# Performance work log

Measured on AMD Instinct MI355X. Metric: run time of the kernel, lower is better.

Reference implementation:

```python
import jax, jax.numpy as jnp
import numpy as np

N = 100000   # nodes
E = 1600000  # edges
H = 128      # hidden_dim
B = 4096     # number of root pairs
HOPS = 3


def setup_inputs() -> dict:
    key = jax.random.key(0)
    ks = jax.random.split(key, 12)
    s = 0.05
    return {
        "node_feat": jax.random.normal(ks[0], (N, H), jnp.float32),
        "send_embd": jax.random.normal(ks[1], (N, H), jnp.float32),
        "edge_index": jax.random.randint(ks[2], (2, E), 0, N, dtype=jnp.int32),
        "root_index": jax.random.randint(ks[3], (2 * B,), 0, N, dtype=jnp.int32),
        "agg_by_source": 1,
        "lin1_W": jax.random.normal(ks[4], (2 * H, H), jnp.float32) * s,
        "lin1_b": jnp.zeros((H,), jnp.float32),
        "gat_W": jax.random.normal(ks[5], (HOPS, H, H), jnp.float32) * s,
        "gat_asrc": jax.random.normal(ks[6], (HOPS, H), jnp.float32) * s,
        "gat_adst": jax.random.normal(ks[7], (HOPS, H), jnp.float32) * s,
        "gat_b": jnp.zeros((HOPS, H), jnp.float32),
        "lstm_Wih": jax.random.normal(ks[8], (HOPS, 2 * H, 4 * H), jnp.float32) * s,
        "lstm_Whh": jax.random.normal(ks[9], (HOPS, H, 4 * H), jnp.float32) * s,
        "lstm_b": jnp.zeros((HOPS, 4 * H), jnp.float32),
        "lin2_W": jax.random.normal(ks[10], (H, H), jnp.float32) * s,
        "lin2_b": jnp.zeros((H,), jnp.float32),
    }


def _gat_breadth(x, src, dst, W, a_src, a_dst, b):
    # GATConv(heads=1) followed by tanh (GeniePath Breadth layer)
    xw = x @ W                                  # [N, H]
    e_score = jax.nn.leaky_relu((xw @ a_src)[src] + (xw @ a_dst)[dst], 0.2)  # [E]
    # softmax over incoming edges of each destination node
    m = jax.ops.segment_max(e_score, dst, num_segments=N)
    ex = jnp.exp(e_score - m[dst])
    z = jax.ops.segment_sum(ex, dst, num_segments=N)
    alpha = ex / z[dst]                          # [E]
    agg = jax.ops.segment_sum(alpha[:, None] * xw[src], dst, num_segments=N)
    return jnp.tanh(agg + b)


def _lstm_step(inp, h, c, Wih, Whh, b):
    gates = inp @ Wih + h @ Whh + b              # [N, 4H]
    i, f, g, o = jnp.split(gates, 4, axis=-1)
    c = jax.nn.sigmoid(f) * c + jax.nn.sigmoid(i) * jnp.tanh(g)
    h = jax.nn.sigmoid(o) * jnp.tanh(c)
    return h, c


def reference(node_feat, send_embd, edge_index, root_index, agg_by_source,
              lin1_W, lin1_b, gat_W, gat_asrc, gat_adst, gat_b,
              lstm_Wih, lstm_Whh, lstm_b, lin2_W, lin2_b):
    src, dst = edge_index[0], edge_index[1]
    # Aggregation stage input: concat node embedding with broadcast embedding
    x = jnp.concatenate([node_feat, send_embd], axis=1) @ lin1_W + lin1_b  # [N, H]
    # GeniePathLazy: all breadth (GAT) layers run on the projected input x
    h_tmps = [
        _gat_breadth(x, src, dst, gat_W[i], gat_asrc[i], gat_adst[i], gat_b[i])
        for i in range(HOPS)
    ]
    # Depth: per-node LSTM over the hop axis, input = cat(h_tmp, x_prev)
    h = jnp.zeros_like(x)
    c = jnp.zeros_like(x)
    xs = x
    for i in range(HOPS):
        inp = jnp.concatenate([h_tmps[i], xs], axis=1)   # [N, 2H]
        h, c = _lstm_step(inp, h, c, lstm_Wih[i], lstm_Whh[i], lstm_b[i])
        xs = h
    out = xs @ lin2_W + lin2_b                            # [N, H]
    roots = root_index.reshape(-1, 2)
    src_nodes = roots[:, 0] if agg_by_source else roots[:, 1]
    return out[src_nodes]                                 # [B, H]
```

## Files before the change

### kernel.cpp

```cpp
#include <hip/hip_runtime.h>

constexpr int N  = 100000;
constexpr int E  = 1600000;
constexpr int H  = 128;
constexpr int NB = 4096;
constexpr int HOPS = 3;
constexpr int EPT = 8;

constexpr int WOFF_L1  = 0;
constexpr int WOFF_GAT = 32768;
constexpr int WOFF_CAT = 81920;
constexpr int WOFF_L2  = 671744;
constexpr int WTOT     = 688128;

constexpr size_t ALIGN = 256;
constexpr size_t alup(size_t x) { return (x + ALIGN - 1) & ~(ALIGN - 1); }

constexpr size_t OFF_X       = 0;
constexpr size_t OFF_SSRC    = alup(OFF_X + (size_t)N * H * 4);
constexpr size_t OFF_SDST    = alup(OFF_SSRC + (size_t)3 * N * 4);
constexpr size_t OFF_WVEC    = alup(OFF_SDST + (size_t)3 * N * 4);
constexpr size_t OFF_SELMAP  = alup(OFF_WVEC + 6 * H * 4);
constexpr size_t OFF_NODELST = alup(OFF_SELMAP + (size_t)N * 4);
constexpr size_t OFF_CNT     = alup(OFF_NODELST + NB * 4);
constexpr size_t OFF_DEG     = alup(OFF_CNT + 256);
constexpr size_t OFF_OFFS    = alup(OFF_DEG + NB * 4);
constexpr size_t OFF_CURSOR  = alup(OFF_OFFS + (NB + 1) * 4);
constexpr size_t OFF_ESORT   = alup(OFF_CURSOR + NB * 4);
constexpr size_t OFF_AGGXH   = alup(OFF_ESORT + (size_t)E * 4);
constexpr size_t OFF_AGGXL   = alup(OFF_AGGXH + (size_t)3 * NB * H * 2);
constexpr size_t OFF_XSH     = alup(OFF_AGGXL + (size_t)3 * NB * H * 2);
constexpr size_t OFF_XSL     = alup(OFF_XSH + (size_t)NB * H * 2);
constexpr size_t OFF_HH      = alup(OFF_XSL + (size_t)NB * H * 2);
constexpr size_t OFF_HL      = alup(OFF_HH + (size_t)NB * H * 2);
constexpr size_t OFF_CBUF    = alup(OFF_HL + (size_t)NB * H * 2);
constexpr size_t OFF_L2OUT   = alup(OFF_CBUF + (size_t)NB * H * 4);
constexpr size_t OFF_WHI     = alup(OFF_L2OUT + (size_t)NB * H * 4);
constexpr size_t OFF_WLO     = alup(OFF_WHI + (size_t)WTOT * 2);

constexpr size_t OFF_AGGRAW  = OFF_X;
constexpr size_t OFF_WV2     = OFF_X + (size_t)16 * 1024 * 1024;
constexpr size_t OFF_C2      = OFF_WV2 + 6 * 256 * 4;

__device__ __forceinline__ float lrelu(float v) { return v > 0.f ? v : 0.2f * v; }
__device__ __forceinline__ float sigmoidf_(float v) { return 1.f / (1.f + __expf(-v)); }

__device__ __forceinline__ unsigned short f2bf(float f) {
  unsigned u = __float_as_uint(f);
  unsigned r = (u + 0x7FFFu + ((u >> 16) & 1u)) >> 16;
  return (unsigned short)r;
}
__device__ __forceinline__ float bf2f(unsigned short h) {
  return __uint_as_float((unsigned)h << 16);
}
__device__ __forceinline__ void split_rne(float f, unsigned short& hi, unsigned short& lo) {
  unsigned short hh = f2bf(f);
  hi = hh;
  lo = f2bf(f - bf2f(hh));
}
__device__ __forceinline__ void split_trunc(float f, short* hi, short* lo) {
  unsigned u = __float_as_uint(f);
  *hi = (short)(u >> 16);
  float r = f - __uint_as_float(u & 0xFFFF0000u);
  *lo = (short)(__float_as_uint(r) >> 16);
}

typedef short bf16x8 __attribute__((ext_vector_type(8)));
typedef float f32x4  __attribute__((ext_vector_type(4)));

#define MFMA3(ACC, AH, AL, BH, BL)                                               \
  ACC = __builtin_amdgcn_mfma_f32_16x16x32_bf16(AH, BH, ACC, 0, 0, 0);           \
  ACC = __builtin_amdgcn_mfma_f32_16x16x32_bf16(AH, BL, ACC, 0, 0, 0);           \
  ACC = __builtin_amdgcn_mfma_f32_16x16x32_bf16(AL, BH, ACC, 0, 0, 0);

__global__ void init_ws(int* __restrict__ sel_map, int* __restrict__ deg,
                        int* __restrict__ cursor, int* __restrict__ cnt,
                        float* __restrict__ cbuf, unsigned short* __restrict__ hh,
                        unsigned short* __restrict__ hl, int* __restrict__ need_flag) {
  int i = blockIdx.x * 256 + threadIdx.x;
  int stride = gridDim.x * 256;
  for (int n = i; n < N; n += stride) { sel_map[n] = -1; need_flag[n] = 0; }
  for (int n = i; n < NB; n += stride) { deg[n] = 0; cursor[n] = 0; }
  if (i < 64) cnt[i] = 0;
  for (int n = i; n < NB * H; n += stride) { cbuf[n] = 0.f; hh[n] = 0; hl[n] = 0; }
}

__global__ void prep_kernel(const float* __restrict__ gat_W,
                            const float* __restrict__ a_src,
                            const float* __restrict__ a_dst,
                            float* __restrict__ wvec,
                            const float* __restrict__ lin1_W,
                            const float* __restrict__ Wih,
                            const float* __restrict__ Whh,
                            const float* __restrict__ lin2_W,
                            unsigned short* __restrict__ whi,
                            unsigned short* __restrict__ wlo) {
  if (blockIdx.x < 6) {
    int i = blockIdx.x >> 1, which = blockIdx.x & 1;
    int k = threadIdx.x;
    __shared__ float av[H];
    if (k < H) av[k] = which ? a_dst[i * H + k] : a_src[i * H + k];
    __syncthreads();
    if (k >= H) return;
    const float* Wr = gat_W + (size_t)i * H * H + (size_t)k * H;
    float s = 0.f;
    #pragma unroll 8
    for (int j = 0; j < H; j++) s = fmaf(Wr[j], av[j], s);
    wvec[(i * 2 + which) * H + k] = s;
    return;
  }
  int idx = (blockIdx.x - 6) * 256 + threadIdx.x;
  if (idx >= WTOT) return;
  float v;
  if (idx < WOFF_GAT) {
    int rel = idx;
    int e = rel & 7, lane = (rel >> 3) & 63, tile = rel >> 9;
    int nl = lane & 15, quad = lane >> 4;
    int c = tile & 7, t = tile >> 3;
    int n = c * 16 + nl, k = t * 32 + quad * 8 + e;
    v = lin1_W[k * 128 + n];
  } else if (idx < WOFF_CAT) {
    int rel = idx - WOFF_GAT;
    int hop = rel / 16384; rel %= 16384;
    int e = rel & 7, lane = (rel >> 3) & 63, tile = rel >> 9;
    int nl = lane & 15, quad = lane >> 4;
    int c = tile & 7, t = tile >> 3;
    int n = c * 16 + nl, k = t * 32 + quad * 8 + e;
    v = gat_W[hop * 16384 + k * 128 + n];
  } else if (idx < WOFF_L2) {
    int rel = idx - WOFF_CAT;
    int hop = rel / 196608; rel %= 196608;
    int e = rel & 7, lane = (rel >> 3) & 63, tile = rel >> 9;
    int nl = lane & 15, quad = lane >> 4;
    int c = tile & 31, t = tile >> 5;
    int ftile = c >> 2, g = c & 3;
    int col = g * 128 + ftile * 16 + nl;
    int k = t * 32 + quad * 8 + e;
    v = (k < 256) ? Wih[hop * 131072 + k * 512 + col]
                  : Whh[hop * 65536 + (k - 256) * 512 + col];
  } else {
    int rel = idx - WOFF_L2;
    int e = rel & 7, lane = (rel >> 3) & 63, tile = rel >> 9;
    int nl = lane & 15, quad = lane >> 4;
    int c = tile & 7, t = tile >> 3;
    int n = c * 16 + nl, k = t * 32 + quad * 8 + e;
    v = lin2_W[k * 128 + n];
  }
  unsigned short hh, ll;
  split_rne(v, hh, ll);
  whi[idx] = hh;
  wlo[idx] = ll;
}

__global__ void prep2_kernel(const float* __restrict__ lin1_W,
                             const float* __restrict__ lin1_b,
                             const float* __restrict__ wvec,
                             float* __restrict__ wv2, float* __restrict__ c2) {
  int v = blockIdx.x;
  int j = threadIdx.x;
  __shared__ float wv[H];
  if (j < H) wv[j] = wvec[v * H + j];
  __syncthreads();
  const float* Wr = lin1_W + (size_t)j * H;
  float s = 0.f;
  #pragma unroll 8
  for (int m = 0; m < H; m++) s = fmaf(Wr[m], wv[m], s);
  wv2[v * 256 + j] = s;
  if (j == 0) {
    float cc = 0.f;
    for (int m = 0; m < H; m++) cc = fmaf(lin1_b[m], wv[m], cc);
    c2[v] = cc;
  }
}

__global__ void roots_assign(const int* __restrict__ root, const int* __restrict__ aggp,
                             int* __restrict__ sel_map, int* __restrict__ node_list,
                             int* __restrict__ cnt, int* __restrict__ need_flag) {
  int b = blockIdx.x * 256 + threadIdx.x;
  if (b >= NB) return;
  int node = root[2 * b + (aggp[0] ? 0 : 1)];
  need_flag[node] = 1;
  int old = atomicCAS(&sel_map[node], -1, -2);
  if (old == -1) {
    int c = atomicAdd(cnt, 1);
    sel_map[node] = c;
    node_list[c] = node;
  }
}

__global__ void count_edges(const int* __restrict__ ei, const int* __restrict__ sel_map,
                            int* __restrict__ deg) {
  const int T = gridDim.x * 256;
  const int base = blockIdx.x * 256 + threadIdx.x;
  int dn[EPT];
  #pragma unroll
  for (int k = 0; k < EPT; k++) {
    int e = base + k * T;
    dn[k] = (e < E) ? ei[E + e] : -1;
  }
  #pragma unroll
  for (int k = 0; k < EPT; k++) {
    if (dn[k] >= 0) dn[k] = sel_map[dn[k]];
  }
  #pragma unroll
  for (int k = 0; k < EPT; k++) {
    if (dn[k] >= 0) atomicAdd(&deg[dn[k]], 1);
  }
}

__global__ __launch_bounds__(1024)
void scan_kernel(const int* __restrict__ deg, int* __restrict__ offs) {
  __shared__ int part[1024];
  int t = threadIdx.x;
  int base = t * 4;
  int v0 = deg[base], v1 = deg[base + 1], v2 = deg[base + 2], v3 = deg[base + 3];
  int s = v0 + v1 + v2 + v3;
  part[t] = s;
  __syncthreads();
  for (int off = 1; off < 1024; off <<= 1) {
    int tmp = (t >= off) ? part[t - off] : 0;
    __syncthreads();
    part[t] += tmp;
    __syncthreads();
  }
  int run = part[t] - s;
  offs[base] = run; run += v0;
  offs[base + 1] = run; run += v1;
  offs[base + 2] = run; run += v2;
  offs[base + 3] = run;
  if (t == 1023) offs[NB] = part[1023];
}

__global__ void scatter_edges2(const int* __restrict__ ei, const int* __restrict__ sel_map,
                               const int* __restrict__ offs, int* __restrict__ cursor,
                               int* __restrict__ es_sorted, int* __restrict__ need_flag) {
  const int T = gridDim.x * 256;
  const int base = blockIdx.x * 256 + threadIdx.x;
  int dn[EPT], sn[EPT];
  #pragma unroll
  for (int k = 0; k < EPT; k++) {
    int e = base + k * T;
    dn[k] = (e < E) ? ei[E + e] : -1;
  }
  #pragma unroll
  for (int k = 0; k < EPT; k++) {
    if (dn[k] >= 0) dn[k] = sel_map[dn[k]];
  }
  #pragma unroll
  for (int k = 0; k < EPT; k++) {
    int e = base + k * T;
    if (dn[k] >= 0) sn[k] = ei[e];
  }
  #pragma unroll
  for (int k = 0; k < EPT; k++) {
    if (dn[k] >= 0) {
      int p = atomicAdd(&cursor[dn[k]], 1);
      es_sorted[offs[dn[k]] + p] = sn[k];
      need_flag[sn[k]] = 1;
    }
  }
}

__global__ void compact_need(const int* __restrict__ need_flag,
                             int* __restrict__ need_list, int* __restrict__ need_cnt) {
  int i = blockIdx.x * 256 + threadIdx.x;
  bool f = (i < N) && (need_flag[i] != 0);
  unsigned long long mask = __ballot(f);
  int lane = threadIdx.x & 63;
  int wcnt = __popcll(mask);
  int base = 0;
  if (lane == 0 && wcnt > 0) base = atomicAdd(need_cnt, wcnt);
  base = __shfl(base, 0);
  if (f) {
    int prefix = __popcll(mask & ((1ull << lane) - 1ull));
    need_list[base + prefix] = i;
  }
}

__global__ __launch_bounds__(256)
void score_pass(const float* __restrict__ a0, const float* __restrict__ a1,
                const float* __restrict__ wv2, const float* __restrict__ c2,
                float* __restrict__ s_src, float* __restrict__ s_dst,
                const int* __restrict__ need_list, const int* __restrict__ need_cnt) {
  const int nneed = need_cnt[0];
  if (blockIdx.x * 16 >= nneed) return;
  __shared__ float Ws[6 * 256];
  __shared__ float C2s[6];
  const int t = threadIdx.x, lane = t & 63, wave = t >> 6;
  const int nl = lane & 15;
  #pragma unroll
  for (int v = 0; v < 6; v++) Ws[v * 256 + t] = wv2[v * 256 + t];
  if (t < 6) C2s[t] = c2[t];
  __syncthreads();

  int r = blockIdx.x * 16 + wave * 4 + (lane >> 4);
  int row = (r < nneed) ? need_list[r] : -1;
  int rc = (row < 0) ? 0 : row;
  const float* src = (nl < 8) ? (a0 + (size_t)rc * H + nl * 16)
                              : (a1 + (size_t)rc * H + (nl - 8) * 16);
  float4 va[4];
  #pragma unroll
  for (int q = 0; q < 4; q++) va[q] = ((const float4*)src)[q];

  float p[6] = {0.f, 0.f, 0.f, 0.f, 0.f, 0.f};
  #pragma unroll
  for (int q = 0; q < 4; q++) {
    float4 v4 = va[q];
    #pragma unroll
    for (int v = 0; v < 6; v++) {
      float4 w4 = *(const float4*)&Ws[v * 256 + nl * 16 + q * 4];
      p[v] = fmaf(v4.x, w4.x, p[v]);
      p[v] = fmaf(v4.y, w4.y, p[v]);
      p[v] = fmaf(v4.z, w4.z, p[v]);
      p[v] = fmaf(v4.w, w4.w, p[v]);
    }
  }
  #pragma unroll
  for (int m = 1; m < 16; m <<= 1)
    #pragma unroll
    for (int v = 0; v < 6; v++) p[v] += __shfl_xor(p[v], m);
  if (nl == 0 && row >= 0) {
    #pragma unroll
    for (int h3 = 0; h3 < 3; h3++) {
      s_src[h3 * N + row] = p[2 * h3 + 0] + C2s[2 * h3 + 0];
      s_dst[h3 * N + row] = p[2 * h3 + 1] + C2s[2 * h3 + 1];
    }
  }
}

__global__ __launch_bounds__(256)
void gat_node_kernel(const int* __restrict__ node_list, const int* __restrict__ cntp,
                     const int* __restrict__ offs, const int* __restrict__ es_sorted,
                     const float* __restrict__ a0, const float* __restrict__ a1,
                     const float* __restrict__ s_src, const float* __restrict__ s_dst,
                     float* __restrict__ agg_raw) {
  int c = blockIdx.x;
  if (c >= cntp[0]) return;
  int t = threadIdx.x;
  int n = node_list[c];
  float sd0 = s_dst[0 * N + n], sd1 = s_dst[1 * N + n], sd2 = s_dst[2 * N + n];
  int e0 = offs[c], e1 = offs[c + 1];
  float m0 = -1e30f, m1 = -1e30f, m2 = -1e30f;
  for (int e = e0 + t; e < e1; e += 256) {
    int s = es_sorted[e];
    m0 = fmaxf(m0, lrelu(s_src[0 * N + s] + sd0));
    m1 = fmaxf(m1, lrelu(s_src[1 * N + s] + sd1));
    m2 = fmaxf(m2, lrelu(s_src[2 * N + s] + sd2));
  }
  __shared__ float red[3][256];
  red[0][t] = m0; red[1][t] = m1; red[2][t] = m2;
  __syncthreads();
  for (int s2 = 128; s2 > 0; s2 >>= 1) {
    if (t < s2) {
      red[0][t] = fmaxf(red[0][t], red[0][t + s2]);
      red[1][t] = fmaxf(red[1][t], red[1][t + s2]);
      red[2][t] = fmaxf(red[2][t], red[2][t + s2]);
    }
    __syncthreads();
  }
  m0 = red[0][0]; m1 = red[1][0]; m2 = red[2][0];
  float u0 = 0.f, u1 = 0.f, u2 = 0.f, z0 = 0.f, z1 = 0.f, z2 = 0.f;
  for (int e = e0; e < e1; e++) {
    int s = es_sorted[e];
    float xs = (t < 128) ? a0[(size_t)s * H + t] : a1[(size_t)s * H + (t - 128)];
    float ex0 = __expf(lrelu(s_src[0 * N + s] + sd0) - m0);
    float ex1 = __expf(lrelu(s_src[1 * N + s] + sd1) - m1);
    float ex2 = __expf(lrelu(s_src[2 * N + s] + sd2) - m2);
    z0 += ex0; z1 += ex1; z2 += ex2;
    u0 = fmaf(ex0, xs, u0); u1 = fmaf(ex1, xs, u1); u2 = fmaf(ex2, xs, u2);
  }
  size_t cb = (size_t)c * 256 + t;
  bool any = e1 > e0;
  agg_raw[0 * ((size_t)NB * 256) + cb] = any ? u0 / z0 : 0.f;
  agg_raw[1 * ((size_t)NB * 256) + cb] = any ? u1 / z1 : 0.f;
  agg_raw[2 * ((size_t)NB * 256) + cb] = any ? u2 / z2 : 0.f;
}

__global__ __launch_bounds__(256)
void gemm_unified(const float* __restrict__ agg_raw,
                  const float* __restrict__ a0, const float* __restrict__ a1,
                  const int* __restrict__ node_list, const int* __restrict__ cntp,
                  const int* __restrict__ offs,
                  const unsigned short* __restrict__ Bth,
                  const unsigned short* __restrict__ Btl,
                  const float* __restrict__ bias,
                  unsigned short* __restrict__ aggxh, unsigned short* __restrict__ aggxl,
                  unsigned short* __restrict__ xsh, unsigned short* __restrict__ xsl) {
  const int t = threadIdx.x, lane = t & 63, wave = t >> 6;
  const int nl = lane & 15, quad = lane >> 4;
  const int rt = blockIdx.x * 64 + wave * 16;
  const int cnt = cntp[0];

  int gr = rt + nl;
  const float *pA, *pB;
  if (gr < 12288) {
    pA = agg_raw + (size_t)gr * 256;
    pB = pA + 128;
  } else {
    int cc = gr - 12288;
    int node = (cc < cnt) ? node_list[cc] : 0;
    pA = a0 + (size_t)node * H;
    pB = a1 + (size_t)node * H;
  }

  f32x4 acc[8];
  #pragma unroll
  for (int c = 0; c < 8; c++) acc[c] = (f32x4){0.f, 0.f, 0.f, 0.f};

  #pragma unroll
  for (int kt = 0; kt < 8; kt++) {
    const float* p = ((kt < 4) ? pA : pB) + (kt & 3) * 32 + quad * 8;
    bf16x8 ahi, alo;
    {
      float4 v0 = *(const float4*)p;
      float4 v1 = *(const float4*)(p + 4);
      float af[8] = {v0.x, v0.y, v0.z, v0.w, v1.x, v1.y, v1.z, v1.w};
      #pragma unroll
      for (int j = 0; j < 8; j++) {
        short h_, l_;
        split_trunc(af[j], &h_, &l_);
        ahi[j] = h_;
        alo[j] = l_;
      }
    }
    #pragma unroll
    for (int c = 0; c < 8; c++) {
      size_t boff = ((size_t)(kt * 8 + c) * 64 + lane) * 8;
      bf16x8 bh = *(const bf16x8*)(Bth + boff);
      bf16x8 bl = *(const bf16x8*)(Btl + boff);
      MFMA3(acc[c], ahi, alo, bh, bl);
    }
  }

  float bv[8];
  #pragma unroll
  for (int c = 0; c < 8; c++) bv[c] = bias[c * 16 + nl];

  #pragma unroll
  for (int r = 0; r < 4; r++) {
    int g2 = rt + quad * 4 + r;
    if (g2 < 12288) {
      int cc = g2 & 4095, h = g2 >> 12;
      bool he = offs[cc + 1] > offs[cc];
      size_t base = (size_t)h * NB * H + (size_t)cc * H;
      #pragma unroll
      for (int c = 0; c < 8; c++) {
        float val = acc[c][r] + (he ? bv[c] : 0.f);
        unsigned short vh, vl;
        split_rne(val, vh, vl);
        aggxh[base + c * 16 + nl] = vh;
        aggxl[base + c * 16 + nl] = vl;
      }
    } else {
      int cc = g2 - 12288;
      size_t base = (size_t)cc * H;
      #pragma unroll
      for (int c = 0; c < 8; c++) {
        float val = acc[c][r] + bv[c];
        unsigned short vh, vl;
        split_rne(val, vh, vl);
        xsh[base + c * 16 + nl] = vh;
        xsl[base + c * 16 + nl] = vl;
      }
    }
  }
}

__global__ __launch_bounds__(256)
void hop_fused(const unsigned short* __restrict__ agh, const unsigned short* __restrict__ agl,
               const unsigned short* __restrict__ gWh, const unsigned short* __restrict__ gWl,
               const float* __restrict__ gbias,
               const unsigned short* __restrict__ x1h, const unsigned short* __restrict__ x1l,
               const unsigned short* __restrict__ CWh, const unsigned short* __restrict__ CWl,
               const float* __restrict__ lbias,
               float* __restrict__ cbuf, unsigned short* __restrict__ hh,
               unsigned short* __restrict__ hl,
               const unsigned short* __restrict__ L2h, const unsigned short* __restrict__ L2l,
               const float* __restrict__ lin2_b, float* __restrict__ l2out, int do_lin2) {
  __shared__ unsigned short Hh[16 * 136];
  __shared__ unsigned short Hl[16 * 136];
  const int t = threadIdx.x, lane = t & 63, wave = t >> 6;
  const int nl = lane & 15, quad = lane >> 4;
  const int r0 = blockIdx.x * 16;

  f32x4 acc1[2];
  #pragma unroll
  for (int j = 0; j < 2; j++) acc1[j] = (f32x4){0.f, 0.f, 0.f, 0.f};
  #pragma unroll
  for (int kt = 0; kt < 4; kt++) {
    size_t aoff = (size_t)(r0 + nl) * H + kt * 32 + quad * 8;
    bf16x8 ah = *(const bf16x8*)(agh + aoff);
    bf16x8 al = *(const bf16x8*)(agl + aoff);
    #pragma unroll
    for (int j = 0; j < 2; j++) {
      size_t boff = ((size_t)(kt * 8 + 2 * wave + j) * 64 + lane) * 8;
      bf16x8 bh = *(const bf16x8*)(gWh + boff);
      bf16x8 bl = *(const bf16x8*)(gWl + boff);
      MFMA3(acc1[j], ah, al, bh, bl);
    }
  }
  #pragma unroll
  for (int j = 0; j < 2; j++) {
    int col = wave * 32 + j * 16 + nl;
    float bv = gbias[col];
    #pragma unroll
    for (int r = 0; r < 4; r++) {
      int rl = quad * 4 + r;
      float v = tanhf(acc1[j][r] + bv);
      unsigned short vh, vl2;
      split_rne(v, vh, vl2);
      Hh[rl * 136 + col] = vh;
      Hl[rl * 136 + col] = vl2;
    }
  }
  __syncthreads();

  f32x4 acc2[8];
  #pragma unroll
  for (int j = 0; j < 8; j++) acc2[j] = (f32x4){0.f, 0.f, 0.f, 0.f};
  for (int kt = 0; kt < 12; kt++) {
    int kk = (kt & 3) * 32 + quad * 8;
    bf16x8 ah, al;
    if (kt < 4) {
      ah = *(const bf16x8*)&Hh[nl * 136 + kk];
      al = *(const bf16x8*)&Hl[nl * 136 + kk];
    } else {
      const unsigned short* ph = (kt < 8) ? x1h : hh;
      const unsigned short* pl = (kt < 8) ? x1l : hl;
      size_t aoff = (size_t)(r0 + nl) * H + kk;
      ah = *(const bf16x8*)(ph + aoff);
      al = *(const bf16x8*)(pl + aoff);
    }
    #pragma unroll
    for (int cc = 0; cc < 8; cc++) {
      size_t boff = ((size_t)(kt * 32 + 8 * wave + cc) * 64 + lane) * 8;
      bf16x8 bh = *(const bf16x8*)(CWh + boff);
      bf16x8 bl = *(const bf16x8*)(CWl + boff);
      MFMA3(acc2[cc], ah, al, bh, bl);
    }
  }
  __syncthreads();

  #pragma unroll
  for (int ft = 0; ft < 2; ft++) {
    int f = (2 * wave + ft) * 16 + nl;
    float b_i = lbias[0 * 128 + f], b_f = lbias[1 * 128 + f];
    float b_g = lbias[2 * 128 + f], b_o = lbias[3 * 128 + f];
    #pragma unroll
    for (int r = 0; r < 4; r++) {
      int rl = quad * 4 + r;
      size_t id = (size_t)(r0 + rl) * H + f;
      float gi = acc2[ft * 4 + 0][r] + b_i;
      float gf = acc2[ft * 4 + 1][r] + b_f;
      float gg = acc2[ft * 4 + 2][r] + b_g;
      float go = acc2[ft * 4 + 3][r] + b_o;
      float cp = cbuf[id];
      float cn = sigmoidf_(gf) * cp + sigmoidf_(gi) * tanhf(gg);
      float hn = sigmoidf_(go) * tanhf(cn);
      cbuf[id] = cn;
      unsigned short vh, vl2;
      split_rne(hn, vh, vl2);
      hh[id] = vh;
      hl[id] = vl2;
      if (do_lin2) { Hh[rl * 136 + f] = vh; Hl[rl * 136 + f] = vl2; }
    }
  }

  if (!do_lin2) return;
  __syncthreads();
  f32x4 acc3[2];
  #pragma unroll
  for (int j = 0; j < 2; j++) acc3[j] = (f32x4){0.f, 0.f, 0.f, 0.f};
  #pragma unroll
  for (int kt = 0; kt < 4; kt++) {
    int kk = kt * 32 + quad * 8;
    bf16x8 ah = *(const bf16x8*)&Hh[nl * 136 + kk];
    bf16x8 al = *(const bf16x8*)&Hl[nl * 136 + kk];
    #pragma unroll
    for (int j = 0; j < 2; j++) {
      size_t boff = ((size_t)(kt * 8 + 2 * wave + j) * 64 + lane) * 8;
      bf16x8 bh = *(const bf16x8*)(L2h + boff);
      bf16x8 bl = *(const bf16x8*)(L2l + boff);
      MFMA3(acc3[j], ah, al, bh, bl);
    }
  }
  #pragma unroll
  for (int j = 0; j < 2; j++) {
    int col = wave * 32 + j * 16 + nl;
    float bv = lin2_b[col];
    #pragma unroll
    for (int r = 0; r < 4; r++) {
      int row = r0 + quad * 4 + r;
      l2out[(size_t)row * H + col] = acc3[j][r] + bv;
    }
  }
}

__global__ void scatter_out(const float* __restrict__ l2out, const int* __restrict__ sel_map,
                            const int* __restrict__ root, const int* __restrict__ aggp,
                            float* __restrict__ out) {
  int id = blockIdx.x * 256 + threadIdx.x;
  if (id >= NB * H) return;
  int b = id >> 7, f = id & 127;
  int node = root[2 * b + (aggp[0] ? 0 : 1)];
  int c = sel_map[node];
  out[id] = l2out[(size_t)c * H + f];
}

extern "C" void kernel_launch(void* const* d_in, const int* in_sizes, int n_in,
                              void* d_out, int out_size, void* d_ws, size_t ws_size,
                              hipStream_t stream) {
  const float* node_feat = (const float*)d_in[0];
  const float* send_embd = (const float*)d_in[1];
  const int*   edge_idx  = (const int*)d_in[2];
  const int*   root_idx  = (const int*)d_in[3];
  const int*   aggp      = (const int*)d_in[4];
  const float* lin1_W    = (const float*)d_in[5];
  const float* lin1_b    = (const float*)d_in[6];
  const float* gat_W     = (const float*)d_in[7];
  const float* gat_asrc  = (const float*)d_in[8];
  const float* gat_adst  = (const float*)d_in[9];
  const float* gat_b     = (const float*)d_in[10];
  const float* lstm_Wih  = (const float*)d_in[11];
  const float* lstm_Whh  = (const float*)d_in[12];
  const float* lstm_b    = (const float*)d_in[13];
  const float* lin2_W    = (const float*)d_in[14];
  const float* lin2_b    = (const float*)d_in[15];
  float* out = (float*)d_out;

  char* ws = (char*)d_ws;
  float* agg_raw = (float*)(ws + OFF_AGGRAW);
  float* wv2     = (float*)(ws + OFF_WV2);
  float* c2      = (float*)(ws + OFF_C2);
  float* s_src   = (float*)(ws + OFF_SSRC);
  float* s_dst   = (float*)(ws + OFF_SDST);
  float* wvec    = (float*)(ws + OFF_WVEC);
  int*   sel_map = (int*)(ws + OFF_SELMAP);
  int*   nodelst = (int*)(ws + OFF_NODELST);
  int*   cnt     = (int*)(ws + OFF_CNT);
  int*   deg     = (int*)(ws + OFF_DEG);
  int*   offs    = (int*)(ws + OFF_OFFS);
  int*   cursor  = (int*)(ws + OFF_CURSOR);
  int*   esort   = (int*)(ws + OFF_ESORT);
  unsigned short* aggxh = (unsigned short*)(ws + OFF_AGGXH);
  unsigned short* aggxl = (unsigned short*)(ws + OFF_AGGXL);
  unsigned short* xsh   = (unsigned short*)(ws + OFF_XSH);
  unsigned short* xsl   = (unsigned short*)(ws + OFF_XSL);
  unsigned short* hh    = (unsigned short*)(ws + OFF_HH);
  unsigned short* hl    = (unsigned short*)(ws + OFF_HL);
  float* cbuf    = (float*)(ws + OFF_CBUF);
  float* l2out   = (float*)(ws + OFF_L2OUT);
  unsigned short* whi = (unsigned short*)(ws + OFF_WHI);
  unsigned short* wlo = (unsigned short*)(ws + OFF_WLO);

  int* need_flag = (int*)(ws + OFF_AGGXH);
  int* need_list = need_flag + N;
  int* need_cnt  = cnt + 1;

  init_ws<<<2048, 256, 0, stream>>>(sel_map, deg, cursor, cnt, cbuf, hh, hl, need_flag);
  prep_kernel<<<6 + (WTOT + 255) / 256, 256, 0, stream>>>(
      gat_W, gat_asrc, gat_adst, wvec, lin1_W, lstm_Wih, lstm_Whh, lin2_W, whi, wlo);
  prep2_kernel<<<6, 256, 0, stream>>>(lin1_W, lin1_b, wvec, wv2, c2);
  roots_assign<<<(NB + 255) / 256, 256, 0, stream>>>(root_idx, aggp, sel_map, nodelst, cnt,
                                                     need_flag);

  const int egrid = (E + 256 * EPT - 1) / (256 * EPT);
  count_edges<<<egrid, 256, 0, stream>>>(edge_idx, sel_map, deg);
  scan_kernel<<<1, 1024, 0, stream>>>(deg, offs);
  scatter_edges2<<<egrid, 256, 0, stream>>>(edge_idx, sel_map, offs, cursor, esort,
                                            need_flag);
  compact_need<<<(N + 255) / 256, 256, 0, stream>>>(need_flag, need_list, need_cnt);

  score_pass<<<(N + 15) / 16, 256, 0, stream>>>(
      node_feat, send_embd, wv2, c2, s_src, s_dst, need_list, need_cnt);

  gat_node_kernel<<<NB, 256, 0, stream>>>(nodelst, cnt, offs, esort,
                                          node_feat, send_embd, s_src, s_dst, agg_raw);

  gemm_unified<<<256, 256, 0, stream>>>(
      agg_raw, node_feat, send_embd, nodelst, cnt, offs,
      whi + WOFF_L1, wlo + WOFF_L1, lin1_b,
      aggxh, aggxl, xsh, xsl);

  for (int i = 0; i < HOPS; i++) {
    const unsigned short* x1h = (i == 0) ? xsh : hh;
    const unsigned short* x1l = (i == 0) ? xsl : hl;
    hop_fused<<<NB / 16, 256, 0, stream>>>(
        aggxh + (size_t)i * NB * H, aggxl + (size_t)i * NB * H,
        whi + WOFF_GAT + i * 16384, wlo + WOFF_GAT + i * 16384,
        gat_b + (size_t)i * H,
        x1h, x1l,
        whi + WOFF_CAT + i * 196608, wlo + WOFF_CAT + i * 196608,
        lstm_b + (size_t)i * 512,
        cbuf, hh, hl,
        whi + WOFF_L2, wlo + WOFF_L2, lin2_b, l2out,
        (i == HOPS - 1) ? 1 : 0);
  }

  scatter_out<<<(NB * H + 255) / 256, 256, 0, stream>>>(l2out, sel_map, root_idx, aggp, out);
}
```

Measured before the change: 387.1 us.

## Fuse all three LSTM hops and lin2 into one kernel with register-resident cell state

Replaces the three per-hop kernel launches with a single 512-thread kernel that loops over the hops. The LSTM cell state stays in registers and the hidden state stays in shared memory, so cbuf, hh and hl no longer round-trip through global memory. This also drops their zero-init from init_ws. Hop 0 skips the h@Whh term because h is zero. The cost is more shared memory, more threads per block and extra syncthreads inside each block.

```diff
diff --git a/kernel.cpp b/kernel.cpp
--- a/kernel.cpp
+++ b/kernel.cpp
@@ -31,10 +31,7 @@
 constexpr size_t OFF_AGGXL   = alup(OFF_AGGXH + (size_t)3 * NB * H * 2);
 constexpr size_t OFF_XSH     = alup(OFF_AGGXL + (size_t)3 * NB * H * 2);
 constexpr size_t OFF_XSL     = alup(OFF_XSH + (size_t)NB * H * 2);
-constexpr size_t OFF_HH      = alup(OFF_XSL + (size_t)NB * H * 2);
-constexpr size_t OFF_HL      = alup(OFF_HH + (size_t)NB * H * 2);
-constexpr size_t OFF_CBUF    = alup(OFF_HL + (size_t)NB * H * 2);
-constexpr size_t OFF_L2OUT   = alup(OFF_CBUF + (size_t)NB * H * 4);
+constexpr size_t OFF_L2OUT   = alup(OFF_XSL + (size_t)NB * H * 2);
 constexpr size_t OFF_WHI     = alup(OFF_L2OUT + (size_t)NB * H * 4);
 constexpr size_t OFF_WLO     = alup(OFF_WHI + (size_t)WTOT * 2);
 
@@ -75,14 +72,12 @@
 
 __global__ void init_ws(int* __restrict__ sel_map, int* __restrict__ deg,
                         int* __restrict__ cursor, int* __restrict__ cnt,
-                        float* __restrict__ cbuf, unsigned short* __restrict__ hh,
-                        unsigned short* __restrict__ hl, int* __restrict__ need_flag) {
+                        int* __restrict__ need_flag) {
   int i = blockIdx.x * 256 + threadIdx.x;
   int stride = gridDim.x * 256;
   for (int n = i; n < N; n += stride) { sel_map[n] = -1; need_flag[n] = 0; }
   for (int n = i; n < NB; n += stride) { deg[n] = 0; cursor[n] = 0; }
   if (i < 64) cnt[i] = 0;
-  for (int n = i; n < NB * H; n += stride) { cbuf[n] = 0.f; hh[n] = 0; hl[n] = 0; }
 }
 
 __global__ void prep_kernel(const float* __restrict__ gat_W,
@@ -466,132 +461,164 @@
   }
 }
 
-__global__ __launch_bounds__(256)
-void hop_fused(const unsigned short* __restrict__ agh, const unsigned short* __restrict__ agl,
-               const unsigned short* __restrict__ gWh, const unsigned short* __restrict__ gWl,
-               const float* __restrict__ gbias,
-               const unsigned short* __restrict__ x1h, const unsigned short* __restrict__ x1l,
-               const unsigned short* __restrict__ CWh, const unsigned short* __restrict__ CWl,
-               const float* __restrict__ lbias,
-               float* __restrict__ cbuf, unsigned short* __restrict__ hh,
-               unsigned short* __restrict__ hl,
-               const unsigned short* __restrict__ L2h, const unsigned short* __restrict__ L2l,
-               const float* __restrict__ lin2_b, float* __restrict__ l2out, int do_lin2) {
-  __shared__ unsigned short Hh[16 * 136];
-  __shared__ unsigned short Hl[16 * 136];
+__global__ __launch_bounds__(512)
+void hops3_fused(const unsigned short* __restrict__ aggxh,
+                 const unsigned short* __restrict__ aggxl,
+                 const unsigned short* __restrict__ xsh,
+                 const unsigned short* __restrict__ xsl,
+                 const unsigned short* __restrict__ gWh_all,
+                 const unsigned short* __restrict__ gWl_all,
+                 const float* __restrict__ gbias_all,
+                 const unsigned short* __restrict__ CWh_all,
+                 const unsigned short* __restrict__ CWl_all,
+                 const float* __restrict__ lbias_all,
+                 const unsigned short* __restrict__ L2h,
+                 const unsigned short* __restrict__ L2l,
+                 const float* __restrict__ lin2_b, float* __restrict__ l2out) {
+  __shared__ unsigned short Ah[16 * 136], Al[16 * 136];
+  __shared__ unsigned short Xh[16 * 136], Xl[16 * 136];
+  __shared__ unsigned short Th[16 * 136], Tl[16 * 136];
+  __shared__ unsigned short Hh[16 * 136], Hl[16 * 136];
   const int t = threadIdx.x, lane = t & 63, wave = t >> 6;
   const int nl = lane & 15, quad = lane >> 4;
   const int r0 = blockIdx.x * 16;
 
-  f32x4 acc1[2];
-  #pragma unroll
-  for (int j = 0; j < 2; j++) acc1[j] = (f32x4){0.f, 0.f, 0.f, 0.f};
-  #pragma unroll
-  for (int kt = 0; kt < 4; kt++) {
-    size_t aoff = (size_t)(r0 + nl) * H + kt * 32 + quad * 8;
-    bf16x8 ah = *(const bf16x8*)(agh + aoff);
-    bf16x8 al = *(const bf16x8*)(agl + aoff);
-    #pragma unroll
-    for (int j = 0; j < 2; j++) {
-      size_t boff = ((size_t)(kt * 8 + 2 * wave + j) * 64 + lane) * 8;
+  for (int i = t; i < 16 * 64; i += 512) {
+    int row = i >> 6, c2 = (i & 63) * 2;
+    *(ushort2*)&Xh[row * 136 + c2] = *(const ushort2*)&xsh[(size_t)(r0 + row) * H + c2];
+    *(ushort2*)&Xl[row * 136 + c2] = *(const ushort2*)&xsl[(size_t)(r0 + row) * H + c2];
+  }
+
+  float creg[4] = {0.f, 0.f, 0.f, 0.f};
+  const int f = wave * 16 + nl;
+
+  f32x4 acc2[4];
+  #pragma unroll
+  for (int hop = 0; hop < 3; hop++) {
+    const unsigned short* agh = aggxh + (size_t)hop * NB * H;
+    const unsigned short* agl = aggxl + (size_t)hop * NB * H;
+    __syncthreads();
+    for (int i = t; i < 16 * 64; i += 512) {
+      int row = i >> 6, c2 = (i & 63) * 2;
+      *(ushort2*)&Ah[row * 136 + c2] = *(const ushort2*)&agh[(size_t)(r0 + row) * H + c2];
+      *(ushort2*)&Al[row * 136 + c2] = *(const ushort2*)&agl[(size_t)(r0 + row) * H + c2];
+    }
+    __syncthreads();
+
+    const unsigned short* gWh = gWh_all + hop * 16384;
+    const unsigned short* gWl = gWl_all + hop * 16384;
+    f32x4 acc1 = (f32x4){0.f, 0.f, 0.f, 0.f};
+    #pragma unroll
+    for (int kt = 0; kt < 4; kt++) {
+      int kk = kt * 32 + quad * 8;
+      bf16x8 ah = *(const bf16x8*)&Ah[nl * 136 + kk];
+      bf16x8 al = *(const bf16x8*)&Al[nl * 136 + kk];
+      size_t boff = ((size_t)(kt * 8 + wave) * 64 + lane) * 8;
       bf16x8 bh = *(const bf16x8*)(gWh + boff);
       bf16x8 bl = *(const bf16x8*)(gWl + boff);
-      MFMA3(acc1[j], ah, al, bh, bl);
-    }
-  }
-  #pragma unroll
-  for (int j = 0; j < 2; j++) {
-    int col = wave * 32 + j * 16 + nl;
-    float bv = gbias[col];
-    #pragma unroll
-    for (int r = 0; r < 4; r++) {
-      int rl = quad * 4 + r;
-      float v = tanhf(acc1[j][r] + bv);
-      unsigned short vh, vl2;
-      split_rne(v, vh, vl2);
-      Hh[rl * 136 + col] = vh;
-      Hl[rl * 136 + col] = vl2;
+      MFMA3(acc1, ah, al, bh, bl);
+    }
+    {
+      float bv = gbias_all[hop * H + f];
+      #pragma unroll
+      for (int r = 0; r < 4; r++) {
+        int rl = quad * 4 + r;
+        float v = tanhf(acc1[r] + bv);
+        unsigned short vh, vl2;
+        split_rne(v, vh, vl2);
+        Th[rl * 136 + f] = vh;
+        Tl[rl * 136 + f] = vl2;
+      }
+    }
+    __syncthreads();
+
+    const unsigned short* CWh = CWh_all + hop * 196608;
+    const unsigned short* CWl = CWl_all + hop * 196608;
+    #pragma unroll
+    for (int g = 0; g < 4; g++) acc2[g] = (f32x4){0.f, 0.f, 0.f, 0.f};
+    #pragma unroll
+    for (int kt = 0; kt < 4; kt++) {
+      int kk = kt * 32 + quad * 8;
+      bf16x8 ah = *(const bf16x8*)&Th[nl * 136 + kk];
+      bf16x8 al = *(const bf16x8*)&Tl[nl * 136 + kk];
+      #pragma unroll
+      for (int g = 0; g < 4; g++) {
+        size_t boff = ((size_t)(kt * 32 + wave * 4 + g) * 64 + lane) * 8;
+        bf16x8 bh = *(const bf16x8*)(CWh + boff);
+        bf16x8 bl = *(const bf16x8*)(CWl + boff);
+        MFMA3(acc2[g], ah, al, bh, bl);
+      }
+    }
+    #pragma unroll
+    for (int kt = 0; kt < 4; kt++) {
+      int kk = kt * 32 + quad * 8;
+      bf16x8 ah, al;
+      if (hop == 0) {
+        ah = *(const bf16x8*)&Xh[nl * 136 + kk];
+        al = *(const bf16x8*)&Xl[nl * 136 + kk];
+      } else {
+        ah = *(const bf16x8*)&Hh[nl * 136 + kk];
+        al = *(const bf16x8*)&Hl[nl * 136 + kk];
+      }
+      #pragma unroll
+      for (int g = 0; g < 4; g++) {
+        size_t boff = ((size_t)((kt + 4) * 32 + wave * 4 + g) * 64 + lane) * 8;
+        bf16x8 bh = *(const bf16x8*)(CWh + boff);
+        bf16x8 bl = *(const bf16x8*)(CWl + boff);
+        MFMA3(acc2[g], ah, al, bh, bl);
+      }
+      if (hop > 0) {
+        #pragma unroll
+        for (int g = 0; g < 4; g++) {
+          size_t boff = ((size_t)((kt + 8) * 32 + wave * 4 + g) * 64 + lane) * 8;
+          bf16x8 bh = *(const bf16x8*)(CWh + boff);
+          bf16x8 bl = *(const bf16x8*)(CWl + boff);
+          MFMA3(acc2[g], ah, al, bh, bl);
+        }
+      }
+    }
+    __syncthreads();
+
+    {
+      const float* lb = lbias_all + hop * 512;
+      float b_i = lb[0 * 128 + f], b_f = lb[1 * 128 + f];
+      float b_g = lb[2 * 128 + f], b_o = lb[3 * 128 + f];
+      #pragma unroll
+      for (int r = 0; r < 4; r++) {
+        int rl = quad * 4 + r;
+        float gi = acc2[0][r] + b_i;
+        float gf = acc2[1][r] + b_f;
+        float gg = acc2[2][r] + b_g;
+        float go = acc2[3][r] + b_o;
+        float cn = sigmoidf_(gf) * creg[r] + sigmoidf_(gi) * tanhf(gg);
+        float hn = sigmoidf_(go) * tanhf(cn);
+        creg[r] = cn;
+        unsigned short vh, vl2;
+        split_rne(hn, vh, vl2);
+        Hh[rl * 136 + f] = vh;
+        Hl[rl * 136 + f] = vl2;
+      }
     }
   }
   __syncthreads();
 
-  f32x4 acc2[8];
-  #pragma unroll
-  for (int j = 0; j < 8; j++) acc2[j] = (f32x4){0.f, 0.f, 0.f, 0.f};
-  for (int kt = 0; kt < 12; kt++) {
-    int kk = (kt & 3) * 32 + quad * 8;
-    bf16x8 ah, al;
-    if (kt < 4) {
-      ah = *(const bf16x8*)&Hh[nl * 136 + kk];
-      al = *(const bf16x8*)&Hl[nl * 136 + kk];
-    } else {
-      const unsigned short* ph = (kt < 8) ? x1h : hh;
-      const unsigned short* pl = (kt < 8) ? x1l : hl;
-      size_t aoff = (size_t)(r0 + nl) * H + kk;
-      ah = *(const bf16x8*)(ph + aoff);
-      al = *(const bf16x8*)(pl + aoff);
-    }
-    #pragma unroll
-    for (int cc = 0; cc < 8; cc++) {
-      size_t boff = ((size_t)(kt * 32 + 8 * wave + cc) * 64 + lane) * 8;
-      bf16x8 bh = *(const bf16x8*)(CWh + boff);
-      bf16x8 bl = *(const bf16x8*)(CWl + boff);
-      MFMA3(acc2[cc], ah, al, bh, bl);
-    }
-  }
-  __syncthreads();
-
-  #pragma unroll
-  for (int ft = 0; ft < 2; ft++) {
-    int f = (2 * wave + ft) * 16 + nl;
-    float b_i = lbias[0 * 128 + f], b_f = lbias[1 * 128 + f];
-    float b_g = lbias[2 * 128 + f], b_o = lbias[3 * 128 + f];
-    #pragma unroll
-    for (int r = 0; r < 4; r++) {
-      int rl = quad * 4 + r;
-      size_t id = (size_t)(r0 + rl) * H + f;
-      float gi = acc2[ft * 4 + 0][r] + b_i;
-      float gf = acc2[ft * 4 + 1][r] + b_f;
-      float gg = acc2[ft * 4 + 2][r] + b_g;
-      float go = acc2[ft * 4 + 3][r] + b_o;
-      float cp = cbuf[id];
-      float cn = sigmoidf_(gf) * cp + sigmoidf_(gi) * tanhf(gg);
-      float hn = sigmoidf_(go) * tanhf(cn);
-      cbuf[id] = cn;
-      unsigned short vh, vl2;
-      split_rne(hn, vh, vl2);
-      hh[id] = vh;
-      hl[id] = vl2;
-      if (do_lin2) { Hh[rl * 136 + f] = vh; Hl[rl * 136 + f] = vl2; }
-    }
-  }
-
-  if (!do_lin2) return;
-  __syncthreads();
-  f32x4 acc3[2];
-  #pragma unroll
-  for (int j = 0; j < 2; j++) acc3[j] = (f32x4){0.f, 0.f, 0.f, 0.f};
+  f32x4 acc3 = (f32x4){0.f, 0.f, 0.f, 0.f};
   #pragma unroll
   for (int kt = 0; kt < 4; kt++) {
     int kk = kt * 32 + quad * 8;
     bf16x8 ah = *(const bf16x8*)&Hh[nl * 136 + kk];
     bf16x8 al = *(const bf16x8*)&Hl[nl * 136 + kk];
-    #pragma unroll
-    for (int j = 0; j < 2; j++) {
-      size_t boff = ((size_t)(kt * 8 + 2 * wave + j) * 64 + lane) * 8;
-      bf16x8 bh = *(const bf16x8*)(L2h + boff);
-      bf16x8 bl = *(const bf16x8*)(L2l + boff);
-      MFMA3(acc3[j], ah, al, bh, bl);
-    }
-  }
-  #pragma unroll
-  for (int j = 0; j < 2; j++) {
-    int col = wave * 32 + j * 16 + nl;
-    float bv = lin2_b[col];
+    size_t boff = ((size_t)(kt * 8 + wave) * 64 + lane) * 8;
+    bf16x8 bh = *(const bf16x8*)(L2h + boff);
+    bf16x8 bl = *(const bf16x8*)(L2l + boff);
+    MFMA3(acc3, ah, al, bh, bl);
+  }
+  {
+    float bv = lin2_b[f];
     #pragma unroll
     for (int r = 0; r < 4; r++) {
       int row = r0 + quad * 4 + r;
-      l2out[(size_t)row * H + col] = acc3[j][r] + bv;
+      l2out[(size_t)row * H + f] = acc3[r] + bv;
     }
   }
 }
@@ -646,9 +673,6 @@
   unsigned short* aggxl = (unsigned short*)(ws + OFF_AGGXL);
   unsigned short* xsh   = (unsigned short*)(ws + OFF_XSH);
   unsigned short* xsl   = (unsigned short*)(ws + OFF_XSL);
-  unsigned short* hh    = (unsigned short*)(ws + OFF_HH);
-  unsigned short* hl    = (unsigned short*)(ws + OFF_HL);
-  float* cbuf    = (float*)(ws + OFF_CBUF);
   float* l2out   = (float*)(ws + OFF_L2OUT);
   unsigned short* whi = (unsigned short*)(ws + OFF_WHI);
   unsigned short* wlo = (unsigned short*)(ws + OFF_WLO);
@@ -657,7 +681,7 @@
   int* need_list = need_flag + N;
   int* need_cnt  = cnt + 1;
 
-  init_ws<<<2048, 256, 0, stream>>>(sel_map, deg, cursor, cnt, cbuf, hh, hl, need_flag);
+  init_ws<<<512, 256, 0, stream>>>(sel_map, deg, cursor, cnt, need_flag);
   prep_kernel<<<6 + (WTOT + 255) / 256, 256, 0, stream>>>(
       gat_W, gat_asrc, gat_adst, wvec, lin1_W, lstm_Wih, lstm_Whh, lin2_W, whi, wlo);
   prep2_kernel<<<6, 256, 0, stream>>>(lin1_W, lin1_b, wvec, wv2, c2);
@@ -682,20 +706,11 @@
       whi + WOFF_L1, wlo + WOFF_L1, lin1_b,
       aggxh, aggxl, xsh, xsl);
 
-  for (int i = 0; i < HOPS; i++) {
-    const unsigned short* x1h = (i == 0) ? xsh : hh;
-    const unsigned short* x1l = (i == 0) ? xsl : hl;
-    hop_fused<<<NB / 16, 256, 0, stream>>>(
-        aggxh + (size_t)i * NB * H, aggxl + (size_t)i * NB * H,
-        whi + WOFF_GAT + i * 16384, wlo + WOFF_GAT + i * 16384,
-        gat_b + (size_t)i * H,
-        x1h, x1l,
-        whi + WOFF_CAT + i * 196608, wlo + WOFF_CAT + i * 196608,
-        lstm_b + (size_t)i * 512,
-        cbuf, hh, hl,
-        whi + WOFF_L2, wlo + WOFF_L2, lin2_b, l2out,
-        (i == HOPS - 1) ? 1 : 0);
-  }
+  hops3_fused<<<NB / 16, 512, 0, stream>>>(
+      aggxh, aggxl, xsh, xsl,
+      whi + WOFF_GAT, wlo + WOFF_GAT, gat_b,
+      whi + WOFF_CAT, wlo + WOFF_CAT, lstm_b,
+      whi + WOFF_L2, wlo + WOFF_L2, lin2_b, l2out);
 
   scatter_out<<<(NB * H + 255) / 256, 256, 0, stream>>>(l2out, sel_map, root_idx, aggp, out);
 }
```

After: 323.8 us. 16.4% less time.
